# Kernel optimization log

Measured on AMD Instinct MI355X. Metric: run time of the kernel, lower is better.

The kernel has to match this reference:

```python
import jax, jax.numpy as jnp
import numpy as np

B, N, C, H = 4, 1024, 1024, 16
D = C // H                      # head_dim = 64
FFH = int(int(C * 4.0) * 2 / 3) # 2730
EPS = 1e-6


def rmsnorm(x, w):
    return w * (x * jax.lax.rsqrt(jnp.mean(x * x, axis=-1, keepdims=True) + EPS))


def setup_inputs() -> dict:
    key = jax.random.key(0)
    ks = jax.random.split(key, 12)
    s = 0.02
    return {
        "x": jax.random.normal(ks[0], (B, N, C), jnp.float32),
        "c": jax.random.normal(ks[1], (B, C), jnp.float32),
        "norm1_w": jnp.ones((C,), jnp.float32),
        "norm2_w": jnp.ones((C,), jnp.float32),
        "qkv_w": jax.random.normal(ks[2], (3 * C, C), jnp.float32) * s,
        "qkv_b": jnp.zeros((3 * C,), jnp.float32),
        "q_norm_w": jnp.ones((D,), jnp.float32),
        "k_norm_w": jnp.ones((D,), jnp.float32),
        "proj_w": jax.random.normal(ks[3], (C, C), jnp.float32) * s,
        "proj_b": jnp.zeros((C,), jnp.float32),
        "w12_w": jax.random.normal(ks[4], (2 * FFH, C), jnp.float32) * s,
        "w12_b": jnp.zeros((2 * FFH,), jnp.float32),
        "w3_w": jax.random.normal(ks[5], (C, FFH), jnp.float32) * s,
        "w3_b": jnp.zeros((C,), jnp.float32),
        "ada_w": jax.random.normal(ks[6], (6 * C, C), jnp.float32) * s,
        "ada_b": jnp.zeros((6 * C,), jnp.float32),
    }


def modulate(x, shift, scale):
    return x * (1.0 + scale[:, None, :]) + shift[:, None, :]


def attention(x, qkv_w, qkv_b, q_norm_w, k_norm_w, proj_w, proj_b):
    qkv = x @ qkv_w.T + qkv_b                       # (B,N,3C)
    qkv = qkv.reshape(B, N, 3, H, D)
    q, k, v = qkv[:, :, 0], qkv[:, :, 1], qkv[:, :, 2]   # (B,N,H,D)
    q = jnp.transpose(q, (0, 2, 1, 3))              # (B,H,N,D)
    k = jnp.transpose(k, (0, 2, 1, 3))
    v = jnp.transpose(v, (0, 2, 1, 3))
    q = rmsnorm(q, q_norm_w)
    k = rmsnorm(k, k_norm_w)
    attn = jnp.einsum("bhnd,bhmd->bhnm", q, k) / jnp.sqrt(jnp.float32(D))
    attn = jax.nn.softmax(attn, axis=-1)
    out = jnp.einsum("bhnm,bhmd->bhnd", attn, v)
    out = jnp.transpose(out, (0, 2, 1, 3)).reshape(B, N, C)
    return out @ proj_w.T + proj_b


def swiglu(x, w12_w, w12_b, w3_w, w3_b):
    x12 = x @ w12_w.T + w12_b                       # (B,N,2*FFH)
    x1, x2 = x12[..., :FFH], x12[..., FFH:]
    h = jax.nn.silu(x1) * x2
    return h @ w3_w.T + w3_b


def reference(x, c, norm1_w, norm2_w, qkv_w, qkv_b, q_norm_w, k_norm_w,
              proj_w, proj_b, w12_w, w12_b, w3_w, w3_b, ada_w, ada_b):
    ada = jax.nn.silu(c) @ ada_w.T + ada_b          # (B,6C)
    s1, g1, b1, s2, g2, b2 = jnp.split(ada, 6, axis=-1)
    a = attention(modulate(rmsnorm(x, norm1_w), s1, g1),
                  qkv_w, qkv_b, q_norm_w, k_norm_w, proj_w, proj_b)
    x = x + b1[:, None, :] * a
    m = swiglu(modulate(rmsnorm(x, norm2_w), s2, g2), w12_w, w12_b, w3_w, w3_b)
    x = x + b2[:, None, :] * m
    return x
```

## Files before the change

### kernel.cpp

```cpp
#include <hip/hip_runtime.h>

typedef short s16x8 __attribute__((ext_vector_type(8)));
typedef short s16x4 __attribute__((ext_vector_type(4)));
typedef float f32x4 __attribute__((ext_vector_type(4)));

#define B_   4
#define N_   1024
#define C_   1024
#define H_   16
#define D_   64
#define FFH_ 2730
#define FFP_ 2752
#define FFI_ 5632

__device__ __forceinline__ short f2bf(float f) {
  unsigned u = __float_as_uint(f);
  u += 0x7fff + ((u >> 16) & 1);
  return (short)(unsigned short)(u >> 16);
}
__device__ __forceinline__ float silu(float x) { return x / (1.f + __expf(-x)); }

__device__ __forceinline__ void gload16(const void* g, void* l) {
  __builtin_amdgcn_global_load_lds(
      (const __attribute__((address_space(1))) unsigned*)g,
      (__attribute__((address_space(3))) unsigned*)l, 16, 0, 0);
}

__global__ void cvt_bf(const float* __restrict__ s, short* __restrict__ d, const int n4) {
  for (int i = blockIdx.x * 256 + threadIdx.x; i < n4; i += gridDim.x * 256) {
    const float4 v = ((const float4*)s)[i];
    s16x4 o;
    o[0] = f2bf(v.x); o[1] = f2bf(v.y); o[2] = f2bf(v.z); o[3] = f2bf(v.w);
    *(s16x4*)(d + (size_t)i * 4) = o;
  }
}

__global__ void cvt_w3(const float* __restrict__ s, short* __restrict__ d) {
  const int col = blockIdx.x * 256 + threadIdx.x;
  const int row = blockIdx.y;
  if (col < FFP_)
    d[(size_t)row * FFP_ + col] = (col < FFH_) ? f2bf(s[(size_t)row * FFH_ + col]) : (short)0;
}

__global__ void cvt_w12i(const float* __restrict__ s, short* __restrict__ d) {
  const int r = blockIdx.y;
  const int cb = threadIdx.x * 4;
  s16x4 o;
  if (r < 2 * FFH_) {
    const int j = (r >> 1) + (r & 1) * FFH_;
    const float4 v = *(const float4*)(s + (size_t)j * 1024 + cb);
    o[0] = f2bf(v.x); o[1] = f2bf(v.y); o[2] = f2bf(v.z); o[3] = f2bf(v.w);
  } else {
    o[0] = 0; o[1] = 0; o[2] = 0; o[3] = 0;
  }
  *(s16x4*)(d + (size_t)r * 1024 + cb) = o;
}

__global__ void ada_gemm(const float* __restrict__ c, const float* __restrict__ aw,
                         const float* __restrict__ ab, float* __restrict__ ada) {
  const int j = blockIdx.x;
  const int l = threadIdx.x;
  float acc[4] = {0.f, 0.f, 0.f, 0.f};
  const float4* wr = (const float4*)(aw + (size_t)j * 1024);
  #pragma unroll
  for (int p = 0; p < 4; ++p) {
    const float4 wv = wr[p * 64 + l];
    #pragma unroll
    for (int b = 0; b < 4; ++b) {
      const float4 cv = ((const float4*)(c + b * 1024))[p * 64 + l];
      acc[b] += silu(cv.x) * wv.x + silu(cv.y) * wv.y + silu(cv.z) * wv.z + silu(cv.w) * wv.w;
    }
  }
  #pragma unroll
  for (int b = 0; b < 4; ++b) {
    float a = acc[b];
    #pragma unroll
    for (int m = 1; m < 64; m <<= 1) a += __shfl_xor(a, m);
    if (l == 0) ada[b * 6144 + j] = a + ab[j];
  }
}

__global__ void rmsmod(const float* __restrict__ x, const float* __restrict__ wn,
                       const float* __restrict__ ada, const int sOff, const int gOff,
                       short* __restrict__ out) {
  const int row = blockIdx.x;
  const int b = row >> 10;
  const int t = threadIdx.x;
  const float4 v = ((const float4*)(x + (size_t)row * 1024))[t];
  float ss = v.x * v.x + v.y * v.y + v.z * v.z + v.w * v.w;
  #pragma unroll
  for (int m = 1; m < 64; m <<= 1) ss += __shfl_xor(ss, m);
  __shared__ float red[4];
  if ((t & 63) == 0) red[t >> 6] = ss;
  __syncthreads();
  const float rs = rsqrtf((red[0] + red[1] + red[2] + red[3]) * (1.f / 1024.f) + 1e-6f);
  const int j = t * 4;
  const float* sp = ada + b * 6144 + sOff + j;
  const float* gp = ada + b * 6144 + gOff + j;
  s16x4 o;
  o[0] = f2bf(v.x * rs * wn[j + 0] * (1.f + gp[0]) + sp[0]);
  o[1] = f2bf(v.y * rs * wn[j + 1] * (1.f + gp[1]) + sp[1]);
  o[2] = f2bf(v.z * rs * wn[j + 2] * (1.f + gp[2]) + sp[2]);
  o[3] = f2bf(v.w * rs * wn[j + 3] * (1.f + gp[3]) + sp[3]);
  *(s16x4*)(out + (size_t)row * 1024 + j) = o;
}

template <int EPI>
__launch_bounds__(256, 2)
__global__ void gemm2ph(const short* __restrict__ A, const short* __restrict__ Bt,
                        const int K,
                        const float* __restrict__ bias,
                        const float* __restrict__ adav,
                        const float* __restrict__ resid,
                        float* __restrict__ outF,
                        short* __restrict__ outB,
                        short* __restrict__ qbO, short* __restrict__ kbO,
                        short* __restrict__ vrO,
                        const float* __restrict__ qnw, const float* __restrict__ knw) {
  __shared__ short As[2][128 * 64];
  __shared__ short Bs[2][128 * 64];
  const int t = threadIdx.x;
  const int l = t & 63;
  const int w = t >> 6;
  const int wr = (w >> 1) * 64, wc = (w & 1) * 64;

  const int nwg = gridDim.x * gridDim.y;
  int lin = blockIdx.y * gridDim.x + blockIdx.x;
  lin = (lin & 7) * (nwg >> 3) + (lin >> 3);
  const int m0 = (lin / gridDim.x) * 128;
  const int n0 = (lin % gridDim.x) * 128;
  const int nT = K >> 6;

  f32x4 acc[4][4];
  const f32x4 z4 = {0.f, 0.f, 0.f, 0.f};
  #pragma unroll
  for (int i = 0; i < 4; ++i)
    #pragma unroll
    for (int j = 0; j < 4; ++j) acc[i][j] = z4;

  const int lr = l >> 3;
  const int lc = (l & 7) ^ lr;
  const short* gAs = A + (size_t)(m0 + w * 32 + lr) * K + lc * 8;
  const short* gBs = Bt + (size_t)(n0 + w * 32 + lr) * K + lc * 8;
  const int wofs = w * 32 * 64;

#define STAGE_(buf, kt)                                                        \
  do {                                                                         \
    const int _ko = (kt) * 64;                                                 \
    _Pragma("unroll") for (int p = 0; p < 4; ++p) {                            \
      gload16(gAs + (size_t)p * 8 * K + _ko, &As[buf][wofs + p * 8 * 64]);     \
      gload16(gBs + (size_t)p * 8 * K + _ko, &Bs[buf][wofs + p * 8 * 64]);     \
    }                                                                          \
  } while (0)

  STAGE_(0, 0);
  __syncthreads();

  for (int kt = 0; kt < nT; ++kt) {
    const int cur = kt & 1;
    if (kt + 1 < nT) STAGE_(cur ^ 1, kt + 1);
    #pragma unroll
    for (int kk = 0; kk < 2; ++kk) {
      const int c16 = kk * 4 + (l >> 4);
      s16x8 af[4], bfr[4];
      #pragma unroll
      for (int mf = 0; mf < 4; ++mf) {
        const int r = wr + mf * 16 + (l & 15);
        af[mf] = *(const s16x8*)&As[cur][r * 64 + ((c16 ^ (r & 7)) << 3)];
      }
      #pragma unroll
      for (int nf = 0; nf < 4; ++nf) {
        const int r = wc + nf * 16 + (l & 15);
        bfr[nf] = *(const s16x8*)&Bs[cur][r * 64 + ((c16 ^ (r & 7)) << 3)];
      }
      __builtin_amdgcn_s_setprio(1);
      #pragma unroll
      for (int mf = 0; mf < 4; ++mf)
        #pragma unroll
        for (int nf = 0; nf < 4; ++nf)
          acc[mf][nf] = __builtin_amdgcn_mfma_f32_16x16x32_bf16(af[mf], bfr[nf], acc[mf][nf], 0, 0, 0);
      __builtin_amdgcn_s_setprio(0);
    }
    __syncthreads();
  }
#undef STAGE_

  if (EPI == 1) {
    const int bIdx = m0 >> 10;
    #pragma unroll
    for (int mf = 0; mf < 4; ++mf) {
      const int row = m0 + wr + mf * 16 + ((l >> 4) << 2);
      #pragma unroll
      for (int nf = 0; nf < 4; ++nf) {
        const int col = n0 + wc + nf * 16 + (l & 15);
        const float bsv = bias[col];
        const float av = adav[bIdx * 6144 + col];
        #pragma unroll
        for (int i = 0; i < 4; ++i) {
          const float v = acc[mf][nf][i] + bsv;
          outF[(size_t)(row + i) * 1024 + col] =
              resid[(size_t)(row + i) * 1024 + col] + av * v;
        }
      }
    }
  }

  if (EPI == 2) {
    const int colB = n0 + wc;
    const int sec = colB >> 10;
    const int hh = (colB >> 6) & 15;
    if (sec < 2) {
      short* dst = sec ? kbO : qbO;
      const float* nw = sec ? knw : qnw;
      const float scl = sec ? 1.f : 0.125f;
      #pragma unroll
      for (int mf = 0; mf < 4; ++mf) {
        #pragma unroll
        for (int i = 0; i < 4; ++i) {
          const int row = m0 + wr + mf * 16 + ((l >> 4) << 2) + i;
          float vv[4];
          float ss = 0.f;
          #pragma unroll
          for (int nf = 0; nf < 4; ++nf) {
            vv[nf] = acc[mf][nf][i] + bias[colB + nf * 16 + (l & 15)];
            ss += vv[nf] * vv[nf];
          }
          ss += __shfl_xor(ss, 1); ss += __shfl_xor(ss, 2);
          ss += __shfl_xor(ss, 4); ss += __shfl_xor(ss, 8);
          const float rs = rsqrtf(ss * (1.f / 64.f) + 1e-6f) * scl;
          const int bb = row >> 10, nn = row & 1023;
          #pragma unroll
          for (int nf = 0; nf < 4; ++nf) {
            const int d = nf * 16 + (l & 15);
            dst[((size_t)(bb * 16 + hh) * 1024 + nn) * 64 + d] = f2bf(vv[nf] * rs * nw[d]);
          }
        }
      }
    } else {
      #pragma unroll
      for (int mf = 0; mf < 4; ++mf)
        #pragma unroll
        for (int nf = 0; nf < 4; ++nf) {
          const int col = colB + nf * 16 + (l & 15);
          const float bsv = bias[col];
          #pragma unroll
          for (int i = 0; i < 4; ++i) {
            const int row = m0 + wr + mf * 16 + ((l >> 4) << 2) + i;
            vrO[(size_t)row * 1024 + (col - 2048)] = f2bf(acc[mf][nf][i] + bsv);
          }
        }
    }
  }

  if (EPI == 3) {
    #pragma unroll
    for (int mf = 0; mf < 4; ++mf) {
      #pragma unroll
      for (int nf = 0; nf < 4; ++nf) {
        const int gc = n0 + wc + nf * 16 + (l & 15);
        const int pc = gc >> 1;
        const bool real = pc < FFH_;
        const float b1 = real ? bias[pc] : 0.f;
        const float b2 = real ? bias[FFH_ + pc] : 0.f;
        #pragma unroll
        for (int i = 0; i < 4; ++i) {
          const float v = acc[mf][nf][i];
          const float prt = __shfl_xor(v, 1);
          if (!(l & 1) && real) {
            const float x1 = v + b1, x2 = prt + b2;
            const int row = m0 + wr + mf * 16 + ((l >> 4) << 2) + i;
            outB[(size_t)row * FFP_ + pc] = f2bf(silu(x1) * x2);
          }
        }
      }
    }
  }
}

__global__ void v_trans(const short* __restrict__ vr, short* __restrict__ vt) {
  __shared__ short ld[64][72];
  const int t = threadIdx.x;
  const int bh = blockIdx.y, b = bh >> 4, h = bh & 15;
  const int n0 = blockIdx.x * 64;
  const int nl = t >> 2, cb = (t & 3) * 16;
  const short* src = vr + (size_t)(b * 1024 + n0 + nl) * 1024 + h * 64 + cb;
  *(s16x8*)&ld[nl][cb] = *(const s16x8*)src;
  *(s16x8*)&ld[nl][cb + 8] = *(const s16x8*)(src + 8);
  __syncthreads();
  const int d = t >> 2, np = (t & 3) * 16;
  short* dst = vt + (size_t)(bh * 64 + d) * 1024 + n0 + np;
  s16x8 o0, o1;
  #pragma unroll
  for (int p = 0; p < 8; ++p) { o0[p] = ld[np + p][d]; o1[p] = ld[np + 8 + p][d]; }
  *(s16x8*)dst = o0;
  *(s16x8*)(dst + 8) = o1;
}

__launch_bounds__(256, 2)
__global__ void attn(const short* __restrict__ qb, const short* __restrict__ kb,
                     const short* __restrict__ vt, short* __restrict__ ob) {
  __shared__ short Ks[64 * 64];
  __shared__ short Vs[64 * 64];
  __shared__ short Pl[4][32 * 64];
  const int t = threadIdx.x, l = t & 63, w = t >> 6;
  const int bh = blockIdx.y, b = bh >> 4, h = bh & 15;
  const int q0 = blockIdx.x * 128 + w * 32;
  const short* qp = qb + (size_t)bh * (N_ * D_);
  const short* kp = kb + (size_t)bh * (N_ * D_);
  const short* vp = vt + (size_t)bh * (D_ * N_);

  s16x8 qf[2][2];
  #pragma unroll
  for (int mf = 0; mf < 2; ++mf)
    #pragma unroll
    for (int kk = 0; kk < 2; ++kk)
      qf[mf][kk] = *(const s16x8*)&qp[(q0 + mf * 16 + (l & 15)) * 64 + kk * 32 + ((l >> 4) * 8)];

  f32x4 aco[2][4];
  float rm[2][4], rl[2][4];
  const f32x4 z4 = {0.f, 0.f, 0.f, 0.f};
  #pragma unroll
  for (int mf = 0; mf < 2; ++mf) {
    #pragma unroll
    for (int nd = 0; nd < 4; ++nd) aco[mf][nd] = z4;
    #pragma unroll
    for (int i = 0; i < 4; ++i) { rm[mf][i] = -1e30f; rl[mf][i] = 0.f; }
  }

  const int sr = t >> 2, sc = (t & 3) * 2;
  s16x8 rk[2], rv[2];
  #pragma unroll
  for (int p = 0; p < 2; ++p) {
    rk[p] = *(const s16x8*)&kp[sr * 64 + (sc + p) * 8];
    rv[p] = *(const s16x8*)&vp[sr * 1024 + (sc + p) * 8];
  }

  for (int kt = 0; kt < 16; ++kt) {
    if (kt) __syncthreads();
    #pragma unroll
    for (int p = 0; p < 2; ++p) {
      const int cs = ((sc + p) ^ (sr & 7)) << 3;
      *(s16x8*)&Ks[sr * 64 + cs] = rk[p];
      *(s16x8*)&Vs[sr * 64 + cs] = rv[p];
    }
    __syncthreads();
    if (kt < 15) {
      const int kv0 = (kt + 1) * 64;
      #pragma unroll
      for (int p = 0; p < 2; ++p) {
        rk[p] = *(const s16x8*)&kp[(kv0 + sr) * 64 + (sc + p) * 8];
        rv[p] = *(const s16x8*)&vp[sr * 1024 + kv0 + (sc + p) * 8];
      }
    }

    f32x4 s[2][4];
    #pragma unroll
    for (int mf = 0; mf < 2; ++mf)
      #pragma unroll
      for (int nf = 0; nf < 4; ++nf) s[mf][nf] = z4;

    #pragma unroll
    for (int kk = 0; kk < 2; ++kk) {
      const int c16 = kk * 4 + (l >> 4);
      s16x8 kf[4];
      #pragma unroll
      for (int nf = 0; nf < 4; ++nf) {
        const int r = nf * 16 + (l & 15);
        kf[nf] = *(const s16x8*)&Ks[r * 64 + ((c16 ^ (r & 7)) << 3)];
      }
      __builtin_amdgcn_s_setprio(1);
      #pragma unroll
      for (int mf = 0; mf < 2; ++mf)
        #pragma unroll
        for (int nf = 0; nf < 4; ++nf)
          s[mf][nf] = __builtin_amdgcn_mfma_f32_16x16x32_bf16(qf[mf][kk], kf[nf], s[mf][nf], 0, 0, 0);
      __builtin_amdgcn_s_setprio(0);
    }

    #pragma unroll
    for (int mf = 0; mf < 2; ++mf) {
      #pragma unroll
      for (int i = 0; i < 4; ++i) {
        float pm = fmaxf(fmaxf(s[mf][0][i], s[mf][1][i]), fmaxf(s[mf][2][i], s[mf][3][i]));
        pm = fmaxf(pm, __shfl_xor(pm, 1));
        pm = fmaxf(pm, __shfl_xor(pm, 2));
        pm = fmaxf(pm, __shfl_xor(pm, 4));
        pm = fmaxf(pm, __shfl_xor(pm, 8));
        const float nm = fmaxf(rm[mf][i], pm);
        const float corr = __expf(rm[mf][i] - nm);
        rm[mf][i] = nm;
        float rs = 0.f;
        #pragma unroll
        for (int nf = 0; nf < 4; ++nf) {
          const float p = __expf(s[mf][nf][i] - nm);
          s[mf][nf][i] = p;
          rs += p;
        }
        rs += __shfl_xor(rs, 1);
        rs += __shfl_xor(rs, 2);
        rs += __shfl_xor(rs, 4);
        rs += __shfl_xor(rs, 8);
        rl[mf][i] = rl[mf][i] * corr + rs;
        #pragma unroll
        for (int nd = 0; nd < 4; ++nd) aco[mf][nd][i] *= corr;
      }
    }

    short* pw = &Pl[w][0];
    #pragma unroll
    for (int mf = 0; mf < 2; ++mf)
      #pragma unroll
      for (int nf = 0; nf < 4; ++nf)
        #pragma unroll
        for (int i = 0; i < 4; ++i) {
          const int row = mf * 16 + ((l >> 4) << 2) + i;
          const int col = nf * 16 + (l & 15);
          pw[row * 64 + (((col >> 3) ^ (row & 7)) << 3) + (col & 7)] = f2bf(s[mf][nf][i]);
        }

    #pragma unroll
    for (int kk = 0; kk < 2; ++kk) {
      const int c16 = kk * 4 + (l >> 4);
      s16x8 vf[4];
      #pragma unroll
      for (int nd = 0; nd < 4; ++nd) {
        const int r = nd * 16 + (l & 15);
        vf[nd] = *(const s16x8*)&Vs[r * 64 + ((c16 ^ (r & 7)) << 3)];
      }
      __builtin_amdgcn_s_setprio(1);
      #pragma unroll
      for (int mf = 0; mf < 2; ++mf) {
        const int pr = mf * 16 + (l & 15);
        const s16x8 pf = *(const s16x8*)&pw[pr * 64 + ((c16 ^ (pr & 7)) << 3)];
        #pragma unroll
        for (int nd = 0; nd < 4; ++nd)
          aco[mf][nd] = __builtin_amdgcn_mfma_f32_16x16x32_bf16(pf, vf[nd], aco[mf][nd], 0, 0, 0);
      }
      __builtin_amdgcn_s_setprio(0);
    }
  }

  #pragma unroll
  for (int mf = 0; mf < 2; ++mf)
    #pragma unroll
    for (int i = 0; i < 4; ++i) {
      const float inv = 1.f / rl[mf][i];
      const int row = q0 + mf * 16 + ((l >> 4) << 2) + i;
      #pragma unroll
      for (int nd = 0; nd < 4; ++nd) {
        const int col = h * 64 + nd * 16 + (l & 15);
        ob[(size_t)(b * 1024 + row) * 1024 + col] = f2bf(aco[mf][nd][i] * inv);
      }
    }
}

extern "C" void kernel_launch(void* const* d_in, const int* in_sizes, int n_in,
                              void* d_out, int out_size, void* d_ws, size_t ws_size,
                              hipStream_t stream) {
  const float* x     = (const float*)d_in[0];
  const float* c     = (const float*)d_in[1];
  const float* n1w   = (const float*)d_in[2];
  const float* n2w   = (const float*)d_in[3];
  const float* qkvw  = (const float*)d_in[4];
  const float* qkvb  = (const float*)d_in[5];
  const float* qnw   = (const float*)d_in[6];
  const float* knw   = (const float*)d_in[7];
  const float* projw = (const float*)d_in[8];
  const float* projb = (const float*)d_in[9];
  const float* w12w  = (const float*)d_in[10];
  const float* w12b  = (const float*)d_in[11];
  const float* w3w   = (const float*)d_in[12];
  const float* w3b   = (const float*)d_in[13];
  const float* adaw  = (const float*)d_in[14];
  const float* adab  = (const float*)d_in[15];
  float* outp = (float*)d_out;

  char* ws = (char*)d_ws;
  size_t off = 0;
  auto alloc = [&](size_t bytes) { void* p = ws + off; off += (bytes + 255) & ~(size_t)255; return p; };
  short* WQKV = (short*)alloc(3072ull * 1024 * 2);
  short* WPROJ = (short*)alloc(1024ull * 1024 * 2);
  short* W12I = (short*)alloc((size_t)FFI_ * 1024 * 2);
  short* W3B  = (short*)alloc(1024ull * FFP_ * 2);
  float* ADA  = (float*)alloc(4ull * 6144 * 4);
  short* H1   = (short*)alloc(4096ull * 1024 * 2);
  short* QBF  = (short*)alloc(64ull * 1024 * 64 * 2);
  short* KBF  = (short*)alloc(64ull * 1024 * 64 * 2);
  short* VROW = (short*)alloc(4096ull * 1024 * 2);
  short* VTB  = (short*)alloc(64ull * 64 * 1024 * 2);
  short* OBF  = (short*)alloc(4096ull * 1024 * 2);
  float* X1   = (float*)alloc(4096ull * 1024 * 4);
  short* H2   = (short*)alloc(4096ull * 1024 * 2);
  short* HB   = (short*)alloc(4096ull * FFP_ * 2);

  cvt_bf<<<2048, 256, 0, stream>>>(qkvw, WQKV, 3072 * 1024 / 4);
  cvt_bf<<<1024, 256, 0, stream>>>(projw, WPROJ, 1024 * 1024 / 4);
  cvt_w12i<<<dim3(1, FFI_), 256, 0, stream>>>(w12w, W12I);
  cvt_w3<<<dim3(11, 1024), 256, 0, stream>>>(w3w, W3B);
  ada_gemm<<<6144, 64, 0, stream>>>(c, adaw, adab, ADA);
  rmsmod<<<4096, 256, 0, stream>>>(x, n1w, ADA, 0, 1024, H1);
  gemm2ph<2><<<dim3(24, 32), 256, 0, stream>>>(H1, WQKV, 1024, qkvb,
      nullptr, nullptr, nullptr, nullptr, QBF, KBF, VROW, qnw, knw);
  v_trans<<<dim3(16, 64), 256, 0, stream>>>(VROW, VTB);
  attn<<<dim3(8, 64), 256, 0, stream>>>(QBF, KBF, VTB, OBF);
  gemm2ph<1><<<dim3(8, 32), 256, 0, stream>>>(OBF, WPROJ, 1024, projb,
      ADA + 2048, x, X1, nullptr, nullptr, nullptr, nullptr, nullptr, nullptr);
  rmsmod<<<4096, 256, 0, stream>>>(X1, n2w, ADA, 3072, 4096, H2);
  gemm2ph<3><<<dim3(FFI_ / 128, 32), 256, 0, stream>>>(H2, W12I, 1024, w12b,
      nullptr, nullptr, nullptr, HB, nullptr, nullptr, nullptr, nullptr, nullptr);
  gemm2ph<1><<<dim3(8, 32), 256, 0, stream>>>(HB, W3B, FFP_, w3b,
      ADA + 5120, X1, outp, nullptr, nullptr, nullptr, nullptr, nullptr, nullptr);
}
```

Measured before the change: 315.5 us.

## Add 256x256-tile 8-wave GEMM with 4-stage pipeline for QKV and W12 projections

Adds a new GEMM kernel with 512 threads, 256x256 output tiles, K-step 32 and a 4-slot LDS ring that prefetches two steps ahead, using explicit vmcnt waits and split A/B staging between MFMA phases. It is used for the QKV and SwiGLU up-projection GEMMs. The W12 weight is repacked so gate and up rows come in interleaved 16-row groups, which lets the SwiGLU epilogue pair accumulators within a lane instead of using a cross-lane shuffle. Larger tiles increase data reuse and reduce global traffic, but they also mean fewer workgroups (192 and 352) on the device, higher register pressure, and an LDS layout without swizzling that may cause bank conflicts.

```diff
diff --git a/kernel.cpp b/kernel.cpp
--- a/kernel.cpp
+++ b/kernel.cpp
@@ -11,7 +11,7 @@
 #define D_   64
 #define FFH_ 2730
 #define FFP_ 2752
-#define FFI_ 5632
+#define FFG_ 5632
 
 __device__ __forceinline__ short f2bf(float f) {
   unsigned u = __float_as_uint(f);
@@ -42,18 +42,19 @@
     d[(size_t)row * FFP_ + col] = (col < FFH_) ? f2bf(s[(size_t)row * FFH_ + col]) : (short)0;
 }
 
-__global__ void cvt_w12i(const float* __restrict__ s, short* __restrict__ d) {
-  const int r = blockIdx.y;
+__global__ void cvt_w12g(const float* __restrict__ s, short* __restrict__ d) {
+  const int R = blockIdx.y;
   const int cb = threadIdx.x * 4;
+  const int g = R >> 5, half = (R >> 4) & 1, wi = R & 15;
+  const int j = g * 16 + wi;
   s16x4 o;
-  if (r < 2 * FFH_) {
-    const int j = (r >> 1) + (r & 1) * FFH_;
-    const float4 v = *(const float4*)(s + (size_t)j * 1024 + cb);
+  if (j < FFH_) {
+    const float4 v = *(const float4*)(s + (size_t)(j + half * FFH_) * 1024 + cb);
     o[0] = f2bf(v.x); o[1] = f2bf(v.y); o[2] = f2bf(v.z); o[3] = f2bf(v.w);
   } else {
     o[0] = 0; o[1] = 0; o[2] = 0; o[3] = 0;
   }
-  *(s16x4*)(d + (size_t)r * 1024 + cb) = o;
+  *(s16x4*)(d + (size_t)R * 1024 + cb) = o;
 }
 
 __global__ void ada_gemm(const float* __restrict__ c, const float* __restrict__ aw,
@@ -106,107 +107,100 @@
 }
 
 template <int EPI>
-__launch_bounds__(256, 2)
-__global__ void gemm2ph(const short* __restrict__ A, const short* __restrict__ Bt,
+__launch_bounds__(512, 1)
+__global__ void gemm8ph(const short* __restrict__ A, const short* __restrict__ Bt,
                         const int K,
                         const float* __restrict__ bias,
-                        const float* __restrict__ adav,
-                        const float* __restrict__ resid,
-                        float* __restrict__ outF,
                         short* __restrict__ outB,
                         short* __restrict__ qbO, short* __restrict__ kbO,
                         short* __restrict__ vrO,
                         const float* __restrict__ qnw, const float* __restrict__ knw) {
-  __shared__ short As[2][128 * 64];
-  __shared__ short Bs[2][128 * 64];
+  __shared__ short Ar[4][256 * 32];
+  __shared__ short Br[4][256 * 32];
   const int t = threadIdx.x;
   const int l = t & 63;
   const int w = t >> 6;
-  const int wr = (w >> 1) * 64, wc = (w & 1) * 64;
+  const int wm = w >> 2;
+  const int wn = w & 3;
 
   const int nwg = gridDim.x * gridDim.y;
   int lin = blockIdx.y * gridDim.x + blockIdx.x;
   lin = (lin & 7) * (nwg >> 3) + (lin >> 3);
-  const int m0 = (lin / gridDim.x) * 128;
-  const int n0 = (lin % gridDim.x) * 128;
-  const int nT = K >> 6;
-
-  f32x4 acc[4][4];
+  const int m0 = (lin / gridDim.x) * 256;
+  const int n0 = (lin % gridDim.x) * 256;
+  const int S = K >> 5;
+
+  f32x4 acc[8][4];
   const f32x4 z4 = {0.f, 0.f, 0.f, 0.f};
   #pragma unroll
-  for (int i = 0; i < 4; ++i)
+  for (int i = 0; i < 8; ++i)
     #pragma unroll
     for (int j = 0; j < 4; ++j) acc[i][j] = z4;
 
-  const int lr = l >> 3;
-  const int lc = (l & 7) ^ lr;
-  const short* gAs = A + (size_t)(m0 + w * 32 + lr) * K + lc * 8;
-  const short* gBs = Bt + (size_t)(n0 + w * 32 + lr) * K + lc * 8;
-  const int wofs = w * 32 * 64;
-
-#define STAGE_(buf, kt)                                                        \
-  do {                                                                         \
-    const int _ko = (kt) * 64;                                                 \
-    _Pragma("unroll") for (int p = 0; p < 4; ++p) {                            \
-      gload16(gAs + (size_t)p * 8 * K + _ko, &As[buf][wofs + p * 8 * 64]);     \
-      gload16(gBs + (size_t)p * 8 * K + _ko, &Bs[buf][wofs + p * 8 * 64]);     \
-    }                                                                          \
-  } while (0)
-
-  STAGE_(0, 0);
-  __syncthreads();
-
-  for (int kt = 0; kt < nT; ++kt) {
-    const int cur = kt & 1;
-    if (kt + 1 < nT) STAGE_(cur ^ 1, kt + 1);
-    #pragma unroll
-    for (int kk = 0; kk < 2; ++kk) {
-      const int c16 = kk * 4 + (l >> 4);
-      s16x8 af[4], bfr[4];
-      #pragma unroll
-      for (int mf = 0; mf < 4; ++mf) {
-        const int r = wr + mf * 16 + (l & 15);
-        af[mf] = *(const s16x8*)&As[cur][r * 64 + ((c16 ^ (r & 7)) << 3)];
-      }
-      #pragma unroll
-      for (int nf = 0; nf < 4; ++nf) {
-        const int r = wc + nf * 16 + (l & 15);
-        bfr[nf] = *(const s16x8*)&Bs[cur][r * 64 + ((c16 ^ (r & 7)) << 3)];
-      }
-      __builtin_amdgcn_s_setprio(1);
-      #pragma unroll
-      for (int mf = 0; mf < 4; ++mf)
-        #pragma unroll
-        for (int nf = 0; nf < 4; ++nf)
-          acc[mf][nf] = __builtin_amdgcn_mfma_f32_16x16x32_bf16(af[mf], bfr[nf], acc[mf][nf], 0, 0, 0);
-      __builtin_amdgcn_s_setprio(0);
-    }
-    __syncthreads();
-  }
-#undef STAGE_
-
-  if (EPI == 1) {
-    const int bIdx = m0 >> 10;
-    #pragma unroll
-    for (int mf = 0; mf < 4; ++mf) {
-      const int row = m0 + wr + mf * 16 + ((l >> 4) << 2);
-      #pragma unroll
-      for (int nf = 0; nf < 4; ++nf) {
-        const int col = n0 + wc + nf * 16 + (l & 15);
-        const float bsv = bias[col];
-        const float av = adav[bIdx * 6144 + col];
-        #pragma unroll
-        for (int i = 0; i < 4; ++i) {
-          const float v = acc[mf][nf][i] + bsv;
-          outF[(size_t)(row + i) * 1024 + col] =
-              resid[(size_t)(row + i) * 1024 + col] + av * v;
-        }
-      }
-    }
-  }
+  const short* aSrc = A + (size_t)(m0 + (l & 15)) * K + (l >> 4) * 8;
+  const short* bSrc = Bt + (size_t)(n0 + (l & 15)) * K + (l >> 4) * 8;
+  const size_t bstep = (size_t)16 * K;
+
+#define STAGE_A(s)                                                             \
+  {                                                                            \
+    const int _sl = (s) & 3;                                                   \
+    gload16(aSrc + (size_t)(2 * w) * bstep + (s) * 32, &Ar[_sl][(2 * w) * 512]); \
+    gload16(aSrc + (size_t)(2 * w + 1) * bstep + (s) * 32, &Ar[_sl][(2 * w + 1) * 512]); \
+  }
+#define STAGE_B(s)                                                             \
+  {                                                                            \
+    const int _sl = (s) & 3;                                                   \
+    gload16(bSrc + (size_t)(2 * w) * bstep + (s) * 32, &Br[_sl][(2 * w) * 512]); \
+    gload16(bSrc + (size_t)(2 * w + 1) * bstep + (s) * 32, &Br[_sl][(2 * w + 1) * 512]); \
+  }
+
+  STAGE_A(0); STAGE_B(0); STAGE_A(1); STAGE_B(1);
+
+  for (int s = 0; s < S; ++s) {
+    const int sl = s & 3;
+    if (s + 1 < S) {
+      asm volatile("s_waitcnt vmcnt(4)" ::: "memory");
+    } else {
+      asm volatile("s_waitcnt vmcnt(0)" ::: "memory");
+    }
+    __builtin_amdgcn_s_barrier();
+    __builtin_amdgcn_sched_barrier(0);
+
+    s16x8 bf[4], af[4];
+    #pragma unroll
+    for (int nf = 0; nf < 4; ++nf)
+      bf[nf] = *(const s16x8*)&Br[sl][(wn * 4 + nf) * 512 + l * 8];
+    #pragma unroll
+    for (int mf = 0; mf < 4; ++mf)
+      af[mf] = *(const s16x8*)&Ar[sl][(wm * 8 + mf) * 512 + l * 8];
+    if (s + 2 < S) STAGE_A(s + 2);
+    __builtin_amdgcn_s_setprio(1);
+    #pragma unroll
+    for (int mf = 0; mf < 4; ++mf)
+      #pragma unroll
+      for (int nf = 0; nf < 4; ++nf)
+        acc[mf][nf] = __builtin_amdgcn_mfma_f32_16x16x32_bf16(af[mf], bf[nf], acc[mf][nf], 0, 0, 0);
+    __builtin_amdgcn_s_setprio(0);
+    __builtin_amdgcn_s_barrier();
+    __builtin_amdgcn_sched_barrier(0);
+
+    #pragma unroll
+    for (int mf = 0; mf < 4; ++mf)
+      af[mf] = *(const s16x8*)&Ar[sl][(wm * 8 + 4 + mf) * 512 + l * 8];
+    if (s + 2 < S) STAGE_B(s + 2);
+    __builtin_amdgcn_s_setprio(1);
+    #pragma unroll
+    for (int mf = 0; mf < 4; ++mf)
+      #pragma unroll
+      for (int nf = 0; nf < 4; ++nf)
+        acc[4 + mf][nf] = __builtin_amdgcn_mfma_f32_16x16x32_bf16(af[mf], bf[nf], acc[4 + mf][nf], 0, 0, 0);
+    __builtin_amdgcn_s_setprio(0);
+  }
+#undef STAGE_A
+#undef STAGE_B
 
   if (EPI == 2) {
-    const int colB = n0 + wc;
+    const int colB = n0 + wn * 64;
     const int sec = colB >> 10;
     const int hh = (colB >> 6) & 15;
     if (sec < 2) {
@@ -214,10 +208,10 @@
       const float* nw = sec ? knw : qnw;
       const float scl = sec ? 1.f : 0.125f;
       #pragma unroll
-      for (int mf = 0; mf < 4; ++mf) {
+      for (int mf = 0; mf < 8; ++mf) {
         #pragma unroll
         for (int i = 0; i < 4; ++i) {
-          const int row = m0 + wr + mf * 16 + ((l >> 4) << 2) + i;
+          const int row = m0 + wm * 128 + mf * 16 + ((l >> 4) << 2) + i;
           float vv[4];
           float ss = 0.f;
           #pragma unroll
@@ -238,14 +232,14 @@
       }
     } else {
       #pragma unroll
-      for (int mf = 0; mf < 4; ++mf)
+      for (int mf = 0; mf < 8; ++mf)
         #pragma unroll
         for (int nf = 0; nf < 4; ++nf) {
           const int col = colB + nf * 16 + (l & 15);
           const float bsv = bias[col];
           #pragma unroll
           for (int i = 0; i < 4; ++i) {
-            const int row = m0 + wr + mf * 16 + ((l >> 4) << 2) + i;
+            const int row = m0 + wm * 128 + mf * 16 + ((l >> 4) << 2) + i;
             vrO[(size_t)row * 1024 + (col - 2048)] = f2bf(acc[mf][nf][i] + bsv);
           }
         }
@@ -254,24 +248,120 @@
 
   if (EPI == 3) {
     #pragma unroll
-    for (int mf = 0; mf < 4; ++mf) {
-      #pragma unroll
-      for (int nf = 0; nf < 4; ++nf) {
-        const int gc = n0 + wc + nf * 16 + (l & 15);
-        const int pc = gc >> 1;
-        const bool real = pc < FFH_;
-        const float b1 = real ? bias[pc] : 0.f;
-        const float b2 = real ? bias[FFH_ + pc] : 0.f;
-        #pragma unroll
-        for (int i = 0; i < 4; ++i) {
-          const float v = acc[mf][nf][i];
-          const float prt = __shfl_xor(v, 1);
-          if (!(l & 1) && real) {
-            const float x1 = v + b1, x2 = prt + b2;
-            const int row = m0 + wr + mf * 16 + ((l >> 4) << 2) + i;
-            outB[(size_t)row * FFP_ + pc] = f2bf(silu(x1) * x2);
+    for (int mf = 0; mf < 8; ++mf) {
+      const int row = m0 + wm * 128 + mf * 16 + ((l >> 4) << 2);
+      #pragma unroll
+      for (int p = 0; p < 2; ++p) {
+        const int rc = (n0 >> 1) + wn * 32 + p * 16 + (l & 15);
+        if (rc < FFP_) {
+          const bool real = rc < FFH_;
+          const float b1 = real ? bias[rc] : 0.f;
+          const float b2 = real ? bias[FFH_ + rc] : 0.f;
+          #pragma unroll
+          for (int i = 0; i < 4; ++i) {
+            float o = 0.f;
+            if (real) {
+              const float x1 = acc[mf][2 * p][i] + b1;
+              const float x2 = acc[mf][2 * p + 1][i] + b2;
+              o = silu(x1) * x2;
+            }
+            outB[(size_t)(row + i) * FFP_ + rc] = f2bf(o);
           }
         }
+      }
+    }
+  }
+}
+
+__launch_bounds__(256, 2)
+__global__ void gemm2ph(const short* __restrict__ A, const short* __restrict__ Bt,
+                        const int K,
+                        const float* __restrict__ bias,
+                        const float* __restrict__ adav,
+                        const float* __restrict__ resid,
+                        float* __restrict__ outF) {
+  __shared__ short As[2][128 * 64];
+  __shared__ short Bs[2][128 * 64];
+  const int t = threadIdx.x;
+  const int l = t & 63;
+  const int w = t >> 6;
+  const int wr = (w >> 1) * 64, wc = (w & 1) * 64;
+
+  const int nwg = gridDim.x * gridDim.y;
+  int lin = blockIdx.y * gridDim.x + blockIdx.x;
+  lin = (lin & 7) * (nwg >> 3) + (lin >> 3);
+  const int m0 = (lin / gridDim.x) * 128;
+  const int n0 = (lin % gridDim.x) * 128;
+  const int nT = K >> 6;
+
+  f32x4 acc[4][4];
+  const f32x4 z4 = {0.f, 0.f, 0.f, 0.f};
+  #pragma unroll
+  for (int i = 0; i < 4; ++i)
+    #pragma unroll
+    for (int j = 0; j < 4; ++j) acc[i][j] = z4;
+
+  const int lr = l >> 3;
+  const int lc = (l & 7) ^ lr;
+  const short* gAs = A + (size_t)(m0 + w * 32 + lr) * K + lc * 8;
+  const short* gBs = Bt + (size_t)(n0 + w * 32 + lr) * K + lc * 8;
+  const int wofs = w * 32 * 64;
+
+#define STAGE_(buf, kt)                                                        \
+  do {                                                                         \
+    const int _ko = (kt) * 64;                                                 \
+    _Pragma("unroll") for (int p = 0; p < 4; ++p) {                            \
+      gload16(gAs + (size_t)p * 8 * K + _ko, &As[buf][wofs + p * 8 * 64]);     \
+      gload16(gBs + (size_t)p * 8 * K + _ko, &Bs[buf][wofs + p * 8 * 64]);     \
+    }                                                                          \
+  } while (0)
+
+  STAGE_(0, 0);
+  __syncthreads();
+
+  for (int kt = 0; kt < nT; ++kt) {
+    const int cur = kt & 1;
+    if (kt + 1 < nT) STAGE_(cur ^ 1, kt + 1);
+    #pragma unroll
+    for (int kk = 0; kk < 2; ++kk) {
+      const int c16 = kk * 4 + (l >> 4);
+      s16x8 af[4], bfr[4];
+      #pragma unroll
+      for (int mf = 0; mf < 4; ++mf) {
+        const int r = wr + mf * 16 + (l & 15);
+        af[mf] = *(const s16x8*)&As[cur][r * 64 + ((c16 ^ (r & 7)) << 3)];
+      }
+      #pragma unroll
+      for (int nf = 0; nf < 4; ++nf) {
+        const int r = wc + nf * 16 + (l & 15);
+        bfr[nf] = *(const s16x8*)&Bs[cur][r * 64 + ((c16 ^ (r & 7)) << 3)];
+      }
+      __builtin_amdgcn_s_setprio(1);
+      #pragma unroll
+      for (int mf = 0; mf < 4; ++mf)
+        #pragma unroll
+        for (int nf = 0; nf < 4; ++nf)
+          acc[mf][nf] = __builtin_amdgcn_mfma_f32_16x16x32_bf16(af[mf], bfr[nf], acc[mf][nf], 0, 0, 0);
+      __builtin_amdgcn_s_setprio(0);
+    }
+    __syncthreads();
+  }
+#undef STAGE_
+
+  const int bIdx = m0 >> 10;
+  #pragma unroll
+  for (int mf = 0; mf < 4; ++mf) {
+    const int row = m0 + wr + mf * 16 + ((l >> 4) << 2);
+    #pragma unroll
+    for (int nf = 0; nf < 4; ++nf) {
+      const int col = n0 + wc + nf * 16 + (l & 15);
+      const float bsv = bias[col];
+      const float av = adav[bIdx * 6144 + col];
+      #pragma unroll
+      for (int i = 0; i < 4; ++i) {
+        const float v = acc[mf][nf][i] + bsv;
+        outF[(size_t)(row + i) * 1024 + col] =
+            resid[(size_t)(row + i) * 1024 + col] + av * v;
       }
     }
   }
@@ -480,7 +570,7 @@
   auto alloc = [&](size_t bytes) { void* p = ws + off; off += (bytes + 255) & ~(size_t)255; return p; };
   short* WQKV = (short*)alloc(3072ull * 1024 * 2);
   short* WPROJ = (short*)alloc(1024ull * 1024 * 2);
-  short* W12I = (short*)alloc((size_t)FFI_ * 1024 * 2);
+  short* W12G = (short*)alloc((size_t)FFG_ * 1024 * 2);
   short* W3B  = (short*)alloc(1024ull * FFP_ * 2);
   float* ADA  = (float*)alloc(4ull * 6144 * 4);
   short* H1   = (short*)alloc(4096ull * 1024 * 2);
@@ -495,19 +585,17 @@
 
   cvt_bf<<<2048, 256, 0, stream>>>(qkvw, WQKV, 3072 * 1024 / 4);
   cvt_bf<<<1024, 256, 0, stream>>>(projw, WPROJ, 1024 * 1024 / 4);
-  cvt_w12i<<<dim3(1, FFI_), 256, 0, stream>>>(w12w, W12I);
+  cvt_w12g<<<dim3(1, FFG_), 256, 0, stream>>>(w12w, W12G);
   cvt_w3<<<dim3(11, 1024), 256, 0, stream>>>(w3w, W3B);
   ada_gemm<<<6144, 64, 0, stream>>>(c, adaw, adab, ADA);
   rmsmod<<<4096, 256, 0, stream>>>(x, n1w, ADA, 0, 1024, H1);
-  gemm2ph<2><<<dim3(24, 32), 256, 0, stream>>>(H1, WQKV, 1024, qkvb,
-      nullptr, nullptr, nullptr, nullptr, QBF, KBF, VROW, qnw, knw);
+  gemm8ph<2><<<dim3(12, 16), 512, 0, stream>>>(H1, WQKV, 1024, qkvb,
+      nullptr, QBF, KBF, VROW, qnw, knw);
   v_trans<<<dim3(16, 64), 256, 0, stream>>>(VROW, VTB);
   attn<<<dim3(8, 64), 256, 0, stream>>>(QBF, KBF, VTB, OBF);
-  gemm2ph<1><<<dim3(8, 32), 256, 0, stream>>>(OBF, WPROJ, 1024, projb,
-      ADA + 2048, x, X1, nullptr, nullptr, nullptr, nullptr, nullptr, nullptr);
+  gemm2ph<<<dim3(8, 32), 256, 0, stream>>>(OBF, WPROJ, 1024, projb, ADA + 2048, x, X1);
   rmsmod<<<4096, 256, 0, stream>>>(X1, n2w, ADA, 3072, 4096, H2);
-  gemm2ph<3><<<dim3(FFI_ / 128, 32), 256, 0, stream>>>(H2, W12I, 1024, w12b,
-      nullptr, nullptr, nullptr, HB, nullptr, nullptr, nullptr, nullptr, nullptr);
-  gemm2ph<1><<<dim3(8, 32), 256, 0, stream>>>(HB, W3B, FFP_, w3b,
-      ADA + 5120, X1, outp, nullptr, nullptr, nullptr, nullptr, nullptr, nullptr);
-}
+  gemm8ph<3><<<dim3(22, 16), 512, 0, stream>>>(H2, W12G, 1024, w12b,
+      HB, nullptr, nullptr, nullptr, nullptr, nullptr);
+  gemm2ph<<<dim3(8, 32), 256, 0, stream>>>(HB, W3B, FFP_, w3b, ADA + 5120, X1, outp);
+}
```

After: 308.4 us. 2.3% less time.
